# Kernel optimization log

Hardware: AMD Instinct MI355X
Metric: run time of the kernel (lower is better)

The kernel has to match this reference:

```python
import jax, jax.numpy as jnp
import numpy as np

B, S, DIN, H, DOUT, E, SEL = 8, 2048, 512, 512, 512, 262144, 512
N = B * S


def setup_inputs() -> dict:
    key = jax.random.key(0)
    ks = jax.random.split(key, 20)
    inp = {
        "x": jax.random.normal(ks[0], (B, S, DIN), dtype=jnp.float32),
        "edge_index": jax.random.randint(ks[1], (2, E), 0, N, dtype=jnp.int64),
        "selected_idx": jax.random.randint(ks[2], (B, SEL), 0, S, dtype=jnp.int64),
        "edge_label": jax.random.randint(ks[3], (E,), 0, 8, dtype=jnp.int64),
    }
    k = 4
    for l, fin in enumerate([DIN, H, H]):
        inp[f"conv{l}_w1"] = jax.random.normal(ks[k], (2 * fin, H), dtype=jnp.float32) * 0.02; k += 1
        inp[f"conv{l}_b1"] = jnp.full((H,), 0.01, dtype=jnp.float32)
        inp[f"conv{l}_w2"] = jax.random.normal(ks[k], (H, H), dtype=jnp.float32) * 0.02; k += 1
        inp[f"conv{l}_b2"] = jnp.full((H,), 0.01, dtype=jnp.float32)
    inp["ffn_w1"] = jax.random.normal(ks[k], (H, H), dtype=jnp.float32) * 0.02; k += 1
    inp["ffn_b1"] = jnp.full((H,), 0.01, dtype=jnp.float32)
    inp["ffn_w2"] = jax.random.normal(ks[k], (H, DOUT), dtype=jnp.float32) * 0.02; k += 1
    inp["ffn_b2"] = jnp.full((DOUT,), 0.01, dtype=jnp.float32)
    return inp


def _ffw(x, w1, b1, w2, b2):
    # FeedForward: fc2(act_dropout(relu(fc1(x)))), dropout=0 in eval
    return jax.nn.relu(x @ w1 + b1) @ w2 + b2


def reference(x, edge_index, selected_idx, edge_label,
              conv0_w1, conv0_b1, conv0_w2, conv0_b2,
              conv1_w1, conv1_b1, conv1_w2, conv1_b2,
              conv2_w1, conv2_b1, conv2_w2, conv2_b2,
              ffn_w1, ffn_b1, ffn_w2, ffn_b2):
    b, s, d = x.shape
    n = b * s
    h = x.reshape(n, d)
    src, dst = edge_index[0], edge_index[1]  # PyG: x_j = source, x_i = target
    convs = [(conv0_w1, conv0_b1, conv0_w2, conv0_b2),
             (conv1_w1, conv1_b1, conv1_w2, conv1_b2),
             (conv2_w1, conv2_b1, conv2_w2, conv2_b2)]
    for w1, b1, w2, b2 in convs:
        xi = h[dst]                                   # [E, F]
        xj = h[src]
        ef = jnp.concatenate([xi, xj - xi], axis=1)   # [E, 2F]
        m = _ffw(ef, w1, b1, w2, b2)                  # per-edge MLP [E, H]
        agg = jax.ops.segment_max(m, dst, num_segments=n)
        agg = jnp.where(jnp.isneginf(agg), 0.0, agg)  # empty segments -> 0 (PyG fill)
        h = jax.nn.relu(agg)                          # dropout p acts as identity in eval
    h = _ffw(h, ffn_w1, ffn_b1, ffn_w2, ffn_b2)
    out = h.reshape(b, s, -1)                         # [B, S, DOUT]
    idx = jnp.broadcast_to(selected_idx[:, :, None], (b, selected_idx.shape[1], out.shape[-1]))
    return jnp.take_along_axis(out, idx, axis=1)      # [B, SEL, DOUT]
```

## Files before the change

kernel.cpp:

```cpp
#include <hip/hip_runtime.h>
#include <hip/hip_bf16.h>


#define N_NODES 16384
#define EDGES   262144
#define HDIM    512
#define SEQ     2048

typedef __attribute__((ext_vector_type(8))) short short8;
typedef __attribute__((ext_vector_type(8))) _Float16 half8;
typedef __attribute__((ext_vector_type(2))) _Float16 half2v;
typedef __attribute__((ext_vector_type(4))) float f32x4;

__device__ __forceinline__ void gld16(const void* g, void* l) {
    __builtin_amdgcn_global_load_lds(
        (const __attribute__((address_space(1))) void*)g,
        (__attribute__((address_space(3))) void*)l, 16, 0, 0);
}
__device__ __forceinline__ unsigned short f2b(float f) {
    unsigned int x = __float_as_uint(f);
    return (unsigned short)((x + 0x7fffu + ((x >> 16) & 1u)) >> 16);
}
__device__ __forceinline__ unsigned short f2h(float f) {
    _Float16 h = (_Float16)f;
    return __builtin_bit_cast(unsigned short, h);
}
__device__ __forceinline__ unsigned int zpack_h(unsigned int u, unsigned int v) {
    half2v a = __builtin_bit_cast(half2v, u);
    half2v b = __builtin_bit_cast(half2v, v);
    half2v s = a + b;
    half2v z = {(_Float16)0.f, (_Float16)0.f};
    half2v r = __builtin_elementwise_max(s, z);
    return __builtin_bit_cast(unsigned int, r);
}
__device__ __forceinline__ short8 frag_ld(const short* S, int row, int q) {
    int p = q ^ ((row >> 1) & 3);
    return *(const short8*)(S + row * 32 + p * 8);
}
__device__ __forceinline__ void stage_tile(const short* G, int kc, short* S, int t) {
#pragma unroll
    for (int it = 0; it < 2; ++it) {
        int lin = it * 256 + t;
        int row = lin >> 2, p = lin & 3;
        int q = p ^ ((row >> 1) & 3);
        gld16(G + (size_t)row * HDIM + kc + q * 8, S + lin * 8);
    }
}
__device__ __forceinline__ void mfma_tile_bf16(const short* As, const short* Bs,
                                               int wm, int wn, int l, f32x4 acc[4][4]) {
    short8 a[4], b[4];
#pragma unroll
    for (int mt = 0; mt < 4; ++mt) a[mt] = frag_ld(As, wm + mt * 16 + (l & 15), l >> 4);
#pragma unroll
    for (int nt = 0; nt < 4; ++nt) b[nt] = frag_ld(Bs, wn + nt * 16 + (l & 15), l >> 4);
#pragma unroll
    for (int mt = 0; mt < 4; ++mt)
#pragma unroll
        for (int nt = 0; nt < 4; ++nt)
            acc[mt][nt] = __builtin_amdgcn_mfma_f32_16x16x32_bf16(a[mt], b[nt], acc[mt][nt], 0, 0, 0);
}
__device__ __forceinline__ half8 frag64(const short* S, int row, int q) {
    int p = q ^ ((row >> 1) & 7) ^ (row & 1);
    return *(const half8*)(S + row * 64 + p * 8);
}
__device__ __forceinline__ void stageB32(const short* __restrict__ Wt, int n0, int col0,
                                         short* buf, int t) {
#pragma unroll
    for (int it = 0; it < 4; ++it) {
        int lin = it * 256 + t;
        int row = lin >> 2, s = lin & 3;
        int q = s ^ ((row >> 1) & 3);
        gld16(Wt + (size_t)(n0 + row) * HDIM + col0 + q * 8, buf + lin * 8);
    }
}

__global__ __launch_bounds__(256) void hist_kernel(
    const int* __restrict__ dst, int* __restrict__ hist) {
    int idx = blockIdx.x * 256 + threadIdx.x;
    atomicAdd(&hist[dst[idx]], 1);
}
__global__ __launch_bounds__(256) void scan_kernel(
    const int* __restrict__ hist, int* __restrict__ cursor) {
    __shared__ int part[256];
    const int t = threadIdx.x, base = t * 64;
    int sum = 0;
    for (int i = 0; i < 64; ++i) sum += hist[base + i];
    part[t] = sum;
    __syncthreads();
    int run = 0;
    for (int i = 0; i < t; ++i) run += part[i];
    for (int i = 0; i < 64; ++i) {
        int h = hist[base + i];
        cursor[base + i] = run;
        run += h;
    }
}
__global__ __launch_bounds__(256) void scatter_kernel(
    const int* __restrict__ dst, const int* __restrict__ src,
    int* __restrict__ cursor, int* __restrict__ dstS, int* __restrict__ srcS) {
    int idx = blockIdx.x * 256 + threadIdx.x;
    int d = dst[idx];
    int p = atomicAdd(&cursor[d], 1);
    dstS[p] = d;
    srcS[p] = src[idx];
}

__global__ __launch_bounds__(256) void prep_weights_kernel(
    const float* __restrict__ w1, const float* __restrict__ w2,
    short* __restrict__ WdT, short* __restrict__ w1bT, short* __restrict__ W2T) {
    __shared__ float tile[32][33];
    const int which = blockIdx.z;
    const int k0 = blockIdx.x * 32, n0 = blockIdx.y * 32;
    const int tx = threadIdx.x, ty = threadIdx.y;
#pragma unroll
    for (int i = 0; i < 4; ++i) {
        int k = k0 + ty + i * 8, n = n0 + tx;
        float v;
        if (which == 0)      v = w1[k * 512 + n] - w1[(k + 512) * 512 + n];
        else if (which == 1) v = w1[(k + 512) * 512 + n];
        else                 v = w2[k * 512 + n];
        tile[ty + i * 8][tx] = v;
    }
    __syncthreads();
    short* out = which == 0 ? WdT : (which == 1 ? w1bT : W2T);
#pragma unroll
    for (int i = 0; i < 4; ++i) {
        int n = n0 + ty + i * 8, k = k0 + tx;
        float v = tile[tx][ty + i * 8];
        out[(size_t)n * 512 + k] = (short)(which == 2 ? f2h(v) : f2b(v));
    }
}
__global__ __launch_bounds__(256) void tr_kernel(
    const float* __restrict__ W1, const float* __restrict__ W2,
    short* __restrict__ T1, short* __restrict__ T2) {
    __shared__ float tile[32][33];
    const float* W = blockIdx.z ? W2 : W1;
    short* T = blockIdx.z ? T2 : T1;
    const int k0 = blockIdx.x * 32, n0 = blockIdx.y * 32;
    const int tx = threadIdx.x, ty = threadIdx.y;
#pragma unroll
    for (int i = 0; i < 4; ++i)
        tile[ty + i * 8][tx] = W[(k0 + ty + i * 8) * 512 + n0 + tx];
    __syncthreads();
#pragma unroll
    for (int i = 0; i < 4; ++i)
        T[(size_t)(n0 + ty + i * 8) * 512 + k0 + tx] = (short)f2b(tile[tx][ty + i * 8]);
}
__global__ __launch_bounds__(256) void cvt_bf16_kernel(
    const float* __restrict__ x, short* __restrict__ xb) {
    int idx = blockIdx.x * 256 + threadIdx.x;
    float4 v = ((const float4*)x)[idx];
    uint2 o;
    o.x = (unsigned int)f2b(v.x) | ((unsigned int)f2b(v.y) << 16);
    o.y = (unsigned int)f2b(v.z) | ((unsigned int)f2b(v.w) << 16);
    ((uint2*)xb)[idx] = o;
}

__global__ __launch_bounds__(256) void node_gemm_uv_kernel(
    const short* __restrict__ A, const short* __restrict__ WdT,
    const short* __restrict__ w1bT, const float* __restrict__ b1,
    short* __restrict__ U, short* __restrict__ V) {
    __shared__ short As[128 * 32];
    __shared__ short Bs[128 * 32];
    const int t = threadIdx.x;
    const int by = blockIdx.y;
    const short* Wt = (by < 4) ? WdT : w1bT;
    short* C = (by < 4) ? U : V;
    const float* bias = (by < 4) ? b1 : nullptr;
    const int m0 = blockIdx.x * 128, n0 = (by & 3) * 128;
    const int w = t >> 6, l = t & 63;
    const int wm = (w & 1) * 64, wn = (w >> 1) * 64;
    f32x4 acc[4][4] = {};
    for (int kc = 0; kc < HDIM; kc += 32) {
        stage_tile(A + (size_t)m0 * HDIM, kc, As, t);
        stage_tile(Wt + (size_t)n0 * HDIM, kc, Bs, t);
        __syncthreads();
        mfma_tile_bf16(As, Bs, wm, wn, l, acc);
        __syncthreads();
    }
#pragma unroll
    for (int mt = 0; mt < 4; ++mt) {
        int m = m0 + wm + mt * 16 + (l >> 4) * 4;
#pragma unroll
        for (int nt = 0; nt < 4; ++nt) {
            int n = n0 + wn + nt * 16 + (l & 15);
            float bv = bias ? bias[n] : 0.f;
#pragma unroll
            for (int r = 0; r < 4; ++r)
                C[(size_t)(m + r) * HDIM + n] = (short)f2h(acc[mt][nt][r] + bv);
        }
    }
}

__device__ __forceinline__ unsigned int fkey(float m) {
    unsigned int b = __float_as_uint(m);
    return ((int)b < 0) ? ~b : (b | 0x80000000u);
}
__device__ __forceinline__ void kflush(unsigned int* K, int d, int col, float m) {
    atomicMax(K + (((size_t)d) << 9) + col, fkey(m));
}
__global__ __launch_bounds__(256, 3) void edge_mfma_kernel(
    const short* __restrict__ U, const short* __restrict__ V,
    const short* __restrict__ Wt, const int* __restrict__ srcS,
    const int* __restrict__ dstS, unsigned int* __restrict__ K) {
    __shared__ short As[64 * 64];
    __shared__ short Bs[2][256 * 32];
    __shared__ int sdst[64], ssrc[64];
    const int t = threadIdx.x;
    const int L  = blockIdx.x;
    const int g  = (L >> 4) * 8 + (L & 7);
    const int nh = (L >> 3) & 1;
    const int e0 = g * 64, n0 = nh * 256;
    if (t < 64) { sdst[t] = dstS[e0 + t]; ssrc[t] = srcS[e0 + t]; }
    __syncthreads();
    const int w = t >> 6, l = t & 63;
    const int wnb = w * 64;
    const int lm = l & 15;
    const int arow = t >> 2, s0 = (t & 3) * 2;
    const int perm = ((arow >> 1) & 7) ^ (arow & 1);
    const int p0 = s0 ^ perm, p1 = (s0 + 1) ^ perm;
    const short* up = U + (((size_t)sdst[arow]) << 9) + s0 * 8;
    const short* vp = V + (((size_t)ssrc[arow]) << 9) + s0 * 8;
    unsigned int* As_u = (unsigned int*)As;
    f32x4 acc[4][4] = {};
    uint4 pu0, pu1, pv0, pv1, nu0, nu1, nv0, nv1;
    stageB32(Wt, n0, 0, Bs[0], t);
    pu0 = *(const uint4*)(up);
    pu1 = *(const uint4*)(up + 8);
    pv0 = *(const uint4*)(vp);
    pv1 = *(const uint4*)(vp + 8);
#pragma unroll
    for (int hh = 0; hh < 16; ++hh) {
        const int kc = (hh >> 1) * 64;
        if (hh < 15) {
            const int c1 = ((hh + 1) >> 1) * 64 + ((hh + 1) & 1) * 32;
            stageB32(Wt, n0, c1, Bs[(hh + 1) & 1], t);
        }
        if ((hh & 1) == 0) {
            if (hh < 14) {
                nu0 = *(const uint4*)(up + kc + 64);
                nu1 = *(const uint4*)(up + kc + 64 + 8);
                nv0 = *(const uint4*)(vp + kc + 64);
                nv1 = *(const uint4*)(vp + kc + 64 + 8);
            }
            uint4 z0, z1;
            z0.x = zpack_h(pu0.x, pv0.x); z0.y = zpack_h(pu0.y, pv0.y);
            z0.z = zpack_h(pu0.z, pv0.z); z0.w = zpack_h(pu0.w, pv0.w);
            z1.x = zpack_h(pu1.x, pv1.x); z1.y = zpack_h(pu1.y, pv1.y);
            z1.z = zpack_h(pu1.z, pv1.z); z1.w = zpack_h(pu1.w, pv1.w);
            *(uint4*)(As_u + arow * 32 + p0 * 4) = z0;
            *(uint4*)(As_u + arow * 32 + p1 * 4) = z1;
        }
        if (hh < 14)       asm volatile("s_waitcnt vmcnt(8) lgkmcnt(0)" ::: "memory");
        else if (hh == 14) asm volatile("s_waitcnt vmcnt(4) lgkmcnt(0)" ::: "memory");
        else               asm volatile("s_waitcnt vmcnt(0) lgkmcnt(0)" ::: "memory");
        __builtin_amdgcn_s_barrier();
        asm volatile("" ::: "memory");
        const short* Bb = Bs[hh & 1];
        const int hq = (hh & 1) * 4 + (l >> 4);
        __builtin_amdgcn_s_setprio(1);
        half8 b[4];
#pragma unroll
        for (int nt = 0; nt < 4; ++nt) {
            int row = wnb + nt * 16 + lm;
            int p = (l >> 4) ^ ((row >> 1) & 3);
            b[nt] = *(const half8*)(Bb + row * 32 + p * 8);
        }
#pragma unroll
        for (int mt = 0; mt < 4; ++mt) {
            half8 a = frag64(As, mt * 16 + lm, hq);
#pragma unroll
            for (int nt = 0; nt < 4; ++nt)
                acc[mt][nt] = __builtin_amdgcn_mfma_f32_16x16x32_f16(a, b[nt], acc[mt][nt], 0, 0, 0);
        }
        __builtin_amdgcn_s_setprio(0);
        if ((hh & 1) == 0 && hh < 14) { pu0 = nu0; pu1 = nu1; pv0 = nv0; pv1 = nv1; }
        asm volatile("" ::: "memory");
        __builtin_amdgcn_s_barrier();
    }
    const int dbase = sdst[0];
    const int drange = sdst[63] - dbase + 1;
    unsigned int* tile = (unsigned int*)Bs[1];
    if (drange <= 16) {
#pragma unroll
        for (int i = 0; i < 16; ++i) tile[i * 256 + t] = 0u;
        __syncthreads();
#pragma unroll
        for (int mt = 0; mt < 4; ++mt) {
            int base = mt * 16 + (l >> 4) * 4;
            int d0 = sdst[base], d1 = sdst[base + 1], d2 = sdst[base + 2], d3 = sdst[base + 3];
            int r0 = d0 - dbase, r1 = d1 - dbase, r2 = d2 - dbase, r3 = d3 - dbase;
#pragma unroll
            for (int nt = 0; nt < 4; ++nt) {
                int colb = wnb + nt * 16 + lm;
                f32x4 a = acc[mt][nt];
                float m = a[0];
                if (d1 == d0) m = fmaxf(m, a[1]);
                else { atomicMax(tile + r0 * 256 + colb, fkey(m)); m = a[1]; }
                if (d2 == d1) m = fmaxf(m, a[2]);
                else { atomicMax(tile + r1 * 256 + colb, fkey(m)); m = a[2]; }
                if (d3 == d2) m = fmaxf(m, a[3]);
                else { atomicMax(tile + r2 * 256 + colb, fkey(m)); m = a[3]; }
                atomicMax(tile + r3 * 256 + colb, fkey(m));
            }
        }
        __syncthreads();
#pragma unroll 4
        for (int r = 0; r < 16; ++r) {
            if (r < drange) {
                unsigned int kv = tile[r * 256 + t];
                if (kv) atomicMax(K + (((size_t)(dbase + r)) << 9) + n0 + t, kv);
            }
        }
    } else {
#pragma unroll
        for (int mt = 0; mt < 4; ++mt) {
            int base = mt * 16 + (l >> 4) * 4;
            int d0 = sdst[base], d1 = sdst[base + 1], d2 = sdst[base + 2], d3 = sdst[base + 3];
#pragma unroll
            for (int nt = 0; nt < 4; ++nt) {
                int col = n0 + wnb + nt * 16 + lm;
                f32x4 a = acc[mt][nt];
                float m = a[0];
                if (d1 == d0) m = fmaxf(m, a[1]); else { kflush(K, d0, col, m); m = a[1]; }
                if (d2 == d1) m = fmaxf(m, a[2]); else { kflush(K, d1, col, m); m = a[2]; }
                if (d3 == d2) m = fmaxf(m, a[3]); else { kflush(K, d2, col, m); m = a[3]; }
                kflush(K, d3, col, m);
            }
        }
    }
}

__global__ __launch_bounds__(256) void decode_kernel(
    unsigned int* __restrict__ K, const float* __restrict__ b2,
    short* __restrict__ hb) {
    int idx = blockIdx.x * 256 + threadIdx.x;
    unsigned int k = K[idx];
    K[idx] = 0u;
    int c = idx & (HDIM - 1);
    float v = 0.f;
    if (k != 0u) {
        unsigned int b = (k & 0x80000000u) ? (k ^ 0x80000000u) : ~k;
        v = __uint_as_float(b) + b2[c];
    }
    hb[idx] = (short)f2b(fmaxf(v, 0.f));
}

__global__ __launch_bounds__(256) void gather_bf16_kernel(
    const short* __restrict__ hb, const int* __restrict__ sel,
    short* __restrict__ hgb) {
    int idx = blockIdx.x * 256 + threadIdx.x;
    int row = idx >> 6, c = idx & 63;
    int b = row >> 9;
    int s = sel[row];
    ((uint4*)hgb)[idx] = ((const uint4*)(hb + (((size_t)(b * SEQ + s)) << 9)))[c];
}

__global__ __launch_bounds__(256) void ffn_gemm_kernel(
    const short* __restrict__ A, const short* __restrict__ Wt,
    const float* __restrict__ bias, short* __restrict__ Cb,
    float* __restrict__ Cf, int relu) {
    __shared__ short As[128 * 32];
    __shared__ short Bs[128 * 32];
    const int t = threadIdx.x;
    const int m0 = blockIdx.x * 128, n0 = blockIdx.y * 128;
    const int w = t >> 6, l = t & 63;
    const int wm = (w & 1) * 64, wn = (w >> 1) * 64;
    f32x4 acc[4][4] = {};
    for (int kc = 0; kc < HDIM; kc += 32) {
        stage_tile(A + (size_t)m0 * HDIM, kc, As, t);
        stage_tile(Wt + (size_t)n0 * HDIM, kc, Bs, t);
        __syncthreads();
        mfma_tile_bf16(As, Bs, wm, wn, l, acc);
        __syncthreads();
    }
#pragma unroll
    for (int mt = 0; mt < 4; ++mt) {
        int m = m0 + wm + mt * 16 + (l >> 4) * 4;
#pragma unroll
        for (int nt = 0; nt < 4; ++nt) {
            int n = n0 + wn + nt * 16 + (l & 15);
            float bv = bias[n];
#pragma unroll
            for (int r = 0; r < 4; ++r) {
                float v = acc[mt][nt][r] + bv;
                if (relu) v = fmaxf(v, 0.f);
                if (Cf) Cf[(size_t)(m + r) * HDIM + n] = v;
                else    Cb[(size_t)(m + r) * HDIM + n] = (short)f2b(v);
            }
        }
    }
}

extern "C" void kernel_launch(void* const* d_in, const int* in_sizes, int n_in,
                              void* d_out, int out_size, void* d_ws, size_t ws_size,
                              hipStream_t stream) {
    const float* x   = (const float*)d_in[0];
    const int*   ei  = (const int*)d_in[1];
    const int*   sel = (const int*)d_in[2];
    const int*   src = ei;
    const int*   dst = ei + EDGES;
    const float* cw1[3] = {(const float*)d_in[4],  (const float*)d_in[8],  (const float*)d_in[12]};
    const float* cb1[3] = {(const float*)d_in[5],  (const float*)d_in[9],  (const float*)d_in[13]};
    const float* cw2[3] = {(const float*)d_in[6],  (const float*)d_in[10], (const float*)d_in[14]};
    const float* cb2[3] = {(const float*)d_in[7],  (const float*)d_in[11], (const float*)d_in[15]};
    const float* fw1 = (const float*)d_in[16];
    const float* fb1 = (const float*)d_in[17];
    const float* fw2 = (const float*)d_in[18];
    const float* fb2 = (const float*)d_in[19];
    float* out = (float*)d_out;

    const size_t MB = 1024 * 1024;
    char* p = (char*)d_ws;
    unsigned int* keys = (unsigned int*)p;
    short* U    = (short*)(p + 32 * MB);
    short* V    = (short*)(p + 48 * MB);
    short* hb   = (short*)(p + 64 * MB);
    short* WdT  = (short*)(p + 80 * MB);
    short* w1bT = WdT + 512 * 512;
    short* W2T  = w1bT + 512 * 512;
    short* fw1T = W2T + 512 * 512;
    short* fw2T = fw1T + 512 * 512;
    int*   dstS = (int*)(p + 83 * MB);
    int*   srcS = (int*)(p + 84 * MB);
    int*   hist = (int*)(p + 85 * MB);
    int*   curs = hist + N_NODES;
    short* hgb  = (short*)(p + 86 * MB);
    short* t1b  = (short*)(p + 90 * MB);

    (void)hipMemsetAsync(hist, 0, N_NODES * sizeof(int), stream);
    hist_kernel<<<EDGES / 256, 256, 0, stream>>>(dst, hist);
    scan_kernel<<<1, 256, 0, stream>>>(hist, curs);
    scatter_kernel<<<EDGES / 256, 256, 0, stream>>>(dst, src, curs, dstS, srcS);

    cvt_bf16_kernel<<<8192, 256, 0, stream>>>(x, hb);
    tr_kernel<<<dim3(16, 16, 2), dim3(32, 8), 0, stream>>>(fw1, fw2, fw1T, fw2T);
    (void)hipMemsetAsync(keys, 0, 32 * MB, stream);

    for (int l = 0; l < 3; ++l) {
        prep_weights_kernel<<<dim3(16, 16, 3), dim3(32, 8), 0, stream>>>(
            cw1[l], cw2[l], WdT, w1bT, W2T);
        node_gemm_uv_kernel<<<dim3(128, 8), 256, 0, stream>>>(hb, WdT, w1bT, cb1[l], U, V);
        edge_mfma_kernel<<<8192, 256, 0, stream>>>(U, V, W2T, srcS, dstS, keys);
        decode_kernel<<<(N_NODES * HDIM) / 256, 256, 0, stream>>>(keys, cb2[l], hb);
    }

    gather_bf16_kernel<<<(4096 * 64) / 256, 256, 0, stream>>>(hb, sel, hgb);
    ffn_gemm_kernel<<<dim3(32, 4), 256, 0, stream>>>(hgb, fw1T, fb1, t1b, nullptr, 1);
    ffn_gemm_kernel<<<dim3(32, 4), 256, 0, stream>>>(t1b, fw2T, fb2, nullptr, out, 0);
}
```

Before: 870.1 us.

## Fuse U/V node GEMMs, vectorize decode, fold gather into FFN GEMM

The node GEMM now computes both U and V in one block, sharing the A tile across two weight tiles, so A is read once instead of twice. It uses twice the accumulators, with launch bounds set to 2 waves per SIMD. The decode kernel processes two keys per thread with vector loads and stores. The selected-row gather is folded into the first FFN GEMM's A-tile load, which removes a kernel and a buffer; the FFN tile shrinks to 64 rows to give more blocks.

```diff
diff --git a/kernel.cpp b/kernel.cpp
--- a/kernel.cpp
+++ b/kernel.cpp
@@ -45,19 +45,6 @@
         int q = p ^ ((row >> 1) & 3);
         gld16(G + (size_t)row * HDIM + kc + q * 8, S + lin * 8);
     }
-}
-__device__ __forceinline__ void mfma_tile_bf16(const short* As, const short* Bs,
-                                               int wm, int wn, int l, f32x4 acc[4][4]) {
-    short8 a[4], b[4];
-#pragma unroll
-    for (int mt = 0; mt < 4; ++mt) a[mt] = frag_ld(As, wm + mt * 16 + (l & 15), l >> 4);
-#pragma unroll
-    for (int nt = 0; nt < 4; ++nt) b[nt] = frag_ld(Bs, wn + nt * 16 + (l & 15), l >> 4);
-#pragma unroll
-    for (int mt = 0; mt < 4; ++mt)
-#pragma unroll
-        for (int nt = 0; nt < 4; ++nt)
-            acc[mt][nt] = __builtin_amdgcn_mfma_f32_16x16x32_bf16(a[mt], b[nt], acc[mt][nt], 0, 0, 0);
 }
 __device__ __forceinline__ half8 frag64(const short* S, int row, int q) {
     int p = q ^ ((row >> 1) & 7) ^ (row & 1);
@@ -156,26 +143,38 @@
     ((uint2*)xb)[idx] = o;
 }
 
-__global__ __launch_bounds__(256) void node_gemm_uv_kernel(
+__global__ __launch_bounds__(256, 2) void node_gemm_uv_kernel(
     const short* __restrict__ A, const short* __restrict__ WdT,
     const short* __restrict__ w1bT, const float* __restrict__ b1,
     short* __restrict__ U, short* __restrict__ V) {
     __shared__ short As[128 * 32];
-    __shared__ short Bs[128 * 32];
+    __shared__ short Bu[128 * 32];
+    __shared__ short Bv[128 * 32];
     const int t = threadIdx.x;
-    const int by = blockIdx.y;
-    const short* Wt = (by < 4) ? WdT : w1bT;
-    short* C = (by < 4) ? U : V;
-    const float* bias = (by < 4) ? b1 : nullptr;
-    const int m0 = blockIdx.x * 128, n0 = (by & 3) * 128;
+    const int m0 = blockIdx.x * 128, n0 = blockIdx.y * 128;
     const int w = t >> 6, l = t & 63;
     const int wm = (w & 1) * 64, wn = (w >> 1) * 64;
-    f32x4 acc[4][4] = {};
+    f32x4 aU[4][4] = {}, aV[4][4] = {};
     for (int kc = 0; kc < HDIM; kc += 32) {
         stage_tile(A + (size_t)m0 * HDIM, kc, As, t);
-        stage_tile(Wt + (size_t)n0 * HDIM, kc, Bs, t);
-        __syncthreads();
-        mfma_tile_bf16(As, Bs, wm, wn, l, acc);
+        stage_tile(WdT + (size_t)n0 * HDIM, kc, Bu, t);
+        stage_tile(w1bT + (size_t)n0 * HDIM, kc, Bv, t);
+        __syncthreads();
+        short8 a[4], bu[4], bv[4];
+#pragma unroll
+        for (int mt = 0; mt < 4; ++mt) a[mt] = frag_ld(As, wm + mt * 16 + (l & 15), l >> 4);
+#pragma unroll
+        for (int nt = 0; nt < 4; ++nt) {
+            bu[nt] = frag_ld(Bu, wn + nt * 16 + (l & 15), l >> 4);
+            bv[nt] = frag_ld(Bv, wn + nt * 16 + (l & 15), l >> 4);
+        }
+#pragma unroll
+        for (int mt = 0; mt < 4; ++mt)
+#pragma unroll
+            for (int nt = 0; nt < 4; ++nt) {
+                aU[mt][nt] = __builtin_amdgcn_mfma_f32_16x16x32_bf16(a[mt], bu[nt], aU[mt][nt], 0, 0, 0);
+                aV[mt][nt] = __builtin_amdgcn_mfma_f32_16x16x32_bf16(a[mt], bv[nt], aV[mt][nt], 0, 0, 0);
+            }
         __syncthreads();
     }
 #pragma unroll
@@ -184,10 +183,12 @@
 #pragma unroll
         for (int nt = 0; nt < 4; ++nt) {
             int n = n0 + wn + nt * 16 + (l & 15);
-            float bv = bias ? bias[n] : 0.f;
-#pragma unroll
-            for (int r = 0; r < 4; ++r)
-                C[(size_t)(m + r) * HDIM + n] = (short)f2h(acc[mt][nt][r] + bv);
+            float bv = b1[n];
+#pragma unroll
+            for (int r = 0; r < 4; ++r) {
+                U[(size_t)(m + r) * HDIM + n] = (short)f2h(aU[mt][nt][r] + bv);
+                V[(size_t)(m + r) * HDIM + n] = (short)f2h(aV[mt][nt][r]);
+            }
         }
     }
 }
@@ -335,47 +336,62 @@
     unsigned int* __restrict__ K, const float* __restrict__ b2,
     short* __restrict__ hb) {
     int idx = blockIdx.x * 256 + threadIdx.x;
-    unsigned int k = K[idx];
-    K[idx] = 0u;
-    int c = idx & (HDIM - 1);
-    float v = 0.f;
-    if (k != 0u) {
-        unsigned int b = (k & 0x80000000u) ? (k ^ 0x80000000u) : ~k;
-        v = __uint_as_float(b) + b2[c];
-    }
-    hb[idx] = (short)f2b(fmaxf(v, 0.f));
-}
-
-__global__ __launch_bounds__(256) void gather_bf16_kernel(
-    const short* __restrict__ hb, const int* __restrict__ sel,
-    short* __restrict__ hgb) {
-    int idx = blockIdx.x * 256 + threadIdx.x;
-    int row = idx >> 6, c = idx & 63;
-    int b = row >> 9;
-    int s = sel[row];
-    ((uint4*)hgb)[idx] = ((const uint4*)(hb + (((size_t)(b * SEQ + s)) << 9)))[c];
+    uint2 k = ((uint2*)K)[idx];
+    uint2 zz = {0u, 0u};
+    ((uint2*)K)[idx] = zz;
+    int c = (idx << 1) & (HDIM - 1);
+    float v0 = 0.f, v1 = 0.f;
+    if (k.x != 0u) {
+        unsigned int b = (k.x & 0x80000000u) ? (k.x ^ 0x80000000u) : ~k.x;
+        v0 = __uint_as_float(b) + b2[c];
+    }
+    if (k.y != 0u) {
+        unsigned int b = (k.y & 0x80000000u) ? (k.y ^ 0x80000000u) : ~k.y;
+        v1 = __uint_as_float(b) + b2[c + 1];
+    }
+    unsigned int o = (unsigned int)f2b(fmaxf(v0, 0.f))
+                   | ((unsigned int)f2b(fmaxf(v1, 0.f)) << 16);
+    ((unsigned int*)hb)[idx] = o;
 }
 
 __global__ __launch_bounds__(256) void ffn_gemm_kernel(
-    const short* __restrict__ A, const short* __restrict__ Wt,
-    const float* __restrict__ bias, short* __restrict__ Cb,
-    float* __restrict__ Cf, int relu) {
-    __shared__ short As[128 * 32];
+    const short* __restrict__ A, const int* __restrict__ sel,
+    const short* __restrict__ Wt, const float* __restrict__ bias,
+    short* __restrict__ Cb, float* __restrict__ Cf, int relu) {
+    __shared__ short As[64 * 32];
     __shared__ short Bs[128 * 32];
     const int t = threadIdx.x;
-    const int m0 = blockIdx.x * 128, n0 = blockIdx.y * 128;
+    const int m0 = blockIdx.x * 64, n0 = blockIdx.y * 128;
     const int w = t >> 6, l = t & 63;
-    const int wm = (w & 1) * 64, wn = (w >> 1) * 64;
-    f32x4 acc[4][4] = {};
+    const int wm = (w & 1) * 32, wn = (w >> 1) * 64;
+    const int srow = t >> 2, sp = t & 3;
+    const int sq = sp ^ ((srow >> 1) & 3);
+    const short* ap;
+    if (sel) {
+        int gr = m0 + srow;
+        ap = A + (((size_t)((gr >> 9) * SEQ + sel[gr])) << 9);
+    } else {
+        ap = A + (size_t)(m0 + srow) * HDIM;
+    }
+    f32x4 acc[2][4] = {};
     for (int kc = 0; kc < HDIM; kc += 32) {
-        stage_tile(A + (size_t)m0 * HDIM, kc, As, t);
+        gld16(ap + kc + sq * 8, As + t * 8);
         stage_tile(Wt + (size_t)n0 * HDIM, kc, Bs, t);
         __syncthreads();
-        mfma_tile_bf16(As, Bs, wm, wn, l, acc);
-        __syncthreads();
-    }
-#pragma unroll
-    for (int mt = 0; mt < 4; ++mt) {
+        short8 a[2], b[4];
+#pragma unroll
+        for (int mt = 0; mt < 2; ++mt) a[mt] = frag_ld(As, wm + mt * 16 + (l & 15), l >> 4);
+#pragma unroll
+        for (int nt = 0; nt < 4; ++nt) b[nt] = frag_ld(Bs, wn + nt * 16 + (l & 15), l >> 4);
+#pragma unroll
+        for (int mt = 0; mt < 2; ++mt)
+#pragma unroll
+            for (int nt = 0; nt < 4; ++nt)
+                acc[mt][nt] = __builtin_amdgcn_mfma_f32_16x16x32_bf16(a[mt], b[nt], acc[mt][nt], 0, 0, 0);
+        __syncthreads();
+    }
+#pragma unroll
+    for (int mt = 0; mt < 2; ++mt) {
         int m = m0 + wm + mt * 16 + (l >> 4) * 4;
 #pragma unroll
         for (int nt = 0; nt < 4; ++nt) {
@@ -425,7 +441,6 @@
     int*   srcS = (int*)(p + 84 * MB);
     int*   hist = (int*)(p + 85 * MB);
     int*   curs = hist + N_NODES;
-    short* hgb  = (short*)(p + 86 * MB);
     short* t1b  = (short*)(p + 90 * MB);
 
     (void)hipMemsetAsync(hist, 0, N_NODES * sizeof(int), stream);
@@ -440,12 +455,11 @@
     for (int l = 0; l < 3; ++l) {
         prep_weights_kernel<<<dim3(16, 16, 3), dim3(32, 8), 0, stream>>>(
             cw1[l], cw2[l], WdT, w1bT, W2T);
-        node_gemm_uv_kernel<<<dim3(128, 8), 256, 0, stream>>>(hb, WdT, w1bT, cb1[l], U, V);
+        node_gemm_uv_kernel<<<dim3(128, 4), 256, 0, stream>>>(hb, WdT, w1bT, cb1[l], U, V);
         edge_mfma_kernel<<<8192, 256, 0, stream>>>(U, V, W2T, srcS, dstS, keys);
-        decode_kernel<<<(N_NODES * HDIM) / 256, 256, 0, stream>>>(keys, cb2[l], hb);
-    }
-
-    gather_bf16_kernel<<<(4096 * 64) / 256, 256, 0, stream>>>(hb, sel, hgb);
-    ffn_gemm_kernel<<<dim3(32, 4), 256, 0, stream>>>(hgb, fw1T, fb1, t1b, nullptr, 1);
-    ffn_gemm_kernel<<<dim3(32, 4), 256, 0, stream>>>(t1b, fw2T, fb2, nullptr, out, 0);
-}
+        decode_kernel<<<(N_NODES * HDIM / 2) / 256, 256, 0, stream>>>(keys, cb2[l], hb);
+    }
+
+    ffn_gemm_kernel<<<dim3(64, 4), 256, 0, stream>>>(hb, sel, fw1T, fb1, t1b, nullptr, 1);
+    ffn_gemm_kernel<<<dim3(64, 4), 256, 0, stream>>>(t1b, nullptr, fw2T, fb2, nullptr, out, 0);
+}
```

After: 845.2 us. 2.9% less time.
